# Optimization experiments

Measured on AMD Instinct MI355X. Metric: run time of the kernel, lower is better.

The kernel has to match this reference:

```python
import jax, jax.numpy as jnp
import numpy as np

B, S, D, H = 2, 2048, 1024, 16
HD = D // H
EPS = 1e-5


def _layernorm(x, g, b):
    mu = jnp.mean(x, axis=-1, keepdims=True)
    var = jnp.mean(jnp.square(x - mu), axis=-1, keepdims=True)
    return (x - mu) * jax.lax.rsqrt(var + EPS) * g + b


def setup_inputs() -> dict:
    key = jax.random.key(0)
    ks = jax.random.split(key, 12)
    s = 1.0 / np.sqrt(D)
    return {
        "x": jax.random.normal(ks[0], (B, S, D), jnp.float32),
        "Wq": jax.random.uniform(ks[1], (D, D), jnp.float32, -s, s),
        "bq": jax.random.uniform(ks[2], (D,), jnp.float32, -s, s),
        "Wk": jax.random.uniform(ks[3], (D, D), jnp.float32, -s, s),
        "bk": jax.random.uniform(ks[4], (D,), jnp.float32, -s, s),
        "Wv": jax.random.uniform(ks[5], (D, D), jnp.float32, -s, s),
        "bv": jax.random.uniform(ks[6], (D,), jnp.float32, -s, s),
        "ln_g": jnp.ones((D,), jnp.float32),
        "ln_b": jnp.zeros((D,), jnp.float32),
        "W1": jax.random.uniform(ks[7], (D, D), jnp.float32, -s, s),
        "b1": jax.random.uniform(ks[8], (D,), jnp.float32, -s, s),
        "W2": jax.random.uniform(ks[9], (D, D), jnp.float32, -s, s),
        "b2": jax.random.uniform(ks[10], (D,), jnp.float32, -s, s),
    }


def reference(x, Wq, bq, Wk, bk, Wv, bv, ln_g, ln_b, W1, b1, W2, b2):
    # QKV projections (torch Linear: x @ W.T + b), split into heads -> [B,H,S,HD]
    q = (x @ Wq.T + bq).reshape(B, S, H, HD).transpose(0, 2, 1, 3)
    k = (x @ Wk.T + bk).reshape(B, S, H, HD).transpose(0, 2, 1, 3)
    v = (x @ Wv.T + bv).reshape(B, S, H, HD).transpose(0, 2, 1, 3)
    # Full score matrix [B,H,S,S] (faithful to unfused original)
    scores = jnp.einsum("bhqd,bhkd->bhqk", q, k) / np.sqrt(HD).astype(np.float32)
    attn = jax.nn.softmax(scores, axis=-1)  # dropout = identity (eval mode)
    ctx = jnp.einsum("bhqk,bhkd->bhqd", attn, v)
    ctx = ctx.transpose(0, 2, 1, 3).reshape(B, S, D)
    ctx = _layernorm(ctx + x, ln_g, ln_b)
    ffn = jax.nn.relu(ctx @ W1.T + b1) @ W2.T + b2
    return _layernorm(ffn + ctx, ln_g, ln_b)
```

## Files before the change

### kernel.cpp

```cpp
#include <hip/hip_runtime.h>
#include <stdint.h>

#define D_MODEL 1024
#define NHEAD   16
#define HDIM    64
#define BATCH   2
#define SEQ     2048
#define NTOK    (BATCH*SEQ)

typedef unsigned short u16;
typedef unsigned int   u32;
typedef __attribute__((ext_vector_type(8)))  short bf16x8;
typedef __attribute__((ext_vector_type(8)))  u16   u16x8;
typedef __attribute__((ext_vector_type(4)))  u16   u16x4;
typedef __attribute__((ext_vector_type(4)))  u32   u32x4;
typedef __attribute__((ext_vector_type(4)))  float f32x4;
typedef __attribute__((ext_vector_type(16))) float f32x16;

#if __has_builtin(__builtin_amdgcn_exp2f)
#define EXP2F __builtin_amdgcn_exp2f
#else
#define EXP2F exp2f
#endif

__device__ __forceinline__ u16 f2bf(float f) {
  uint32_t u = __float_as_uint(f);
  u += 0x7fffu + ((u >> 16) & 1u);
  return (u16)(u >> 16);
}

__device__ __forceinline__ void gl_lds16(const u16* g, u16* l) {
  __builtin_amdgcn_global_load_lds(
      (const __attribute__((address_space(1))) void*)g,
      (__attribute__((address_space(3))) void*)l, 16, 0, 0);
}

__device__ __forceinline__ u32 cvtpk(float lo, float hi) {
  u32 r;
  asm("v_cvt_pk_bf16_f32 %0, %1, %2" : "=v"(r) : "v"(lo), "v"(hi));
  return r;
}
__device__ __forceinline__ void pl32swap(u32& a, u32& b) {
  asm("v_permlane32_swap_b32 %0, %1" : "+v"(a), "+v"(b));
}

__device__ __forceinline__ f32x16 mfma32(bf16x8 a, bf16x8 b, f32x16 c) {
  return __builtin_amdgcn_mfma_f32_32x32x16_bf16(a, b, c, 0, 0, 0);
}

__global__ __launch_bounds__(256) void cvt_all(
    const float* __restrict__ x,  const float* __restrict__ Wq,
    const float* __restrict__ Wk, const float* __restrict__ Wv,
    const float* __restrict__ W1, const float* __restrict__ W2,
    const float* __restrict__ bq, const float* __restrict__ bk,
    const float* __restrict__ bv,
    u16* __restrict__ x_bf, u16* __restrict__ wqkv,
    u16* __restrict__ w1b,  u16* __restrict__ w2b,
    float* __restrict__ bqkv) {
  const int bid = blockIdx.x, t = threadIdx.x;
  if (bid == 4608) {
    for (int i = t; i < 3072; i += 256)
      bqkv[i] = i < 1024 ? bq[i] : (i < 2048 ? bk[i - 1024] : bv[i - 2048]);
    return;
  }
  const float* src; u16* dst; int off;
  if (bid < 2048)      { src = x;  dst = x_bf;            off = bid; }
  else if (bid < 2560) { src = Wq; dst = wqkv;            off = bid - 2048; }
  else if (bid < 3072) { src = Wk; dst = wqkv + (1 << 20); off = bid - 2560; }
  else if (bid < 3584) { src = Wv; dst = wqkv + (2 << 20); off = bid - 3072; }
  else if (bid < 4096) { src = W1; dst = w1b;             off = bid - 3584; }
  else                 { src = W2; dst = w2b;             off = bid - 4096; }
  const int i = (off * 256 + t) * 8;
  float4 a = *(const float4*)(src + i);
  float4 b = *(const float4*)(src + i + 4);
  u16x8 o;
  o[0] = f2bf(a.x); o[1] = f2bf(a.y); o[2] = f2bf(a.z); o[3] = f2bf(a.w);
  o[4] = f2bf(b.x); o[5] = f2bf(b.y); o[6] = f2bf(b.z); o[7] = f2bf(b.w);
  *(u16x8*)(dst + i) = o;
}

template <int EPI>
__global__ __launch_bounds__(256) void gemm_bt(const u16* __restrict__ A,
                                               const u16* __restrict__ B,
                                               const float* __restrict__ bias,
                                               void* __restrict__ C,
                                               int M, int N, int K) {
  __shared__ u16 a_lds[128 * 32];
  __shared__ u16 b_lds[128 * 32];
  const int t = threadIdx.x;
  const int l = t & 63;
  const int w = t >> 6;
  const int wr = w >> 1, wc = w & 1;
  const int gxn = N >> 7;
  const int cpx = gridDim.x >> 3;
  const int swz = (blockIdx.x & 7) * cpx + (blockIdx.x >> 3);
  const int bm = (swz / gxn) * 128, bn = (swz % gxn) * 128;
  const int fl = l & 15, fh = l >> 4;

  f32x4 acc[4][4] = {};

  const int row0 = t >> 2;
  const int row1 = (t + 256) >> 2;
  const int col0 = (t & 3) * 8;

  for (int k0 = 0; k0 < K; k0 += 32) {
    __syncthreads();
    gl_lds16(A + (size_t)(bm + row0) * K + k0 + col0, &a_lds[t * 8]);
    gl_lds16(A + (size_t)(bm + row1) * K + k0 + col0, &a_lds[(t + 256) * 8]);
    gl_lds16(B + (size_t)(bn + row0) * K + k0 + col0, &b_lds[t * 8]);
    gl_lds16(B + (size_t)(bn + row1) * K + k0 + col0, &b_lds[(t + 256) * 8]);
    __syncthreads();

    bf16x8 af[4], bf[4];
#pragma unroll
    for (int mi = 0; mi < 4; ++mi)
      af[mi] = *(const bf16x8*)&a_lds[(wr * 64 + mi * 16 + fl) * 32 + fh * 8];
#pragma unroll
    for (int ni = 0; ni < 4; ++ni)
      bf[ni] = *(const bf16x8*)&b_lds[(wc * 64 + ni * 16 + fl) * 32 + fh * 8];
#pragma unroll
    for (int mi = 0; mi < 4; ++mi)
#pragma unroll
      for (int ni = 0; ni < 4; ++ni)
        acc[mi][ni] = __builtin_amdgcn_mfma_f32_16x16x32_bf16(
            af[mi], bf[ni], acc[mi][ni], 0, 0, 0);
  }

#pragma unroll
  for (int mi = 0; mi < 4; ++mi) {
#pragma unroll
    for (int ni = 0; ni < 4; ++ni) {
      const int col = bn + wc * 64 + ni * 16 + fl;
      const float bv = bias ? bias[col] : 0.f;
#pragma unroll
      for (int r = 0; r < 4; ++r) {
        const int row = bm + wr * 64 + mi * 16 + fh * 4 + r;
        float v = acc[mi][ni][r] + bv;
        if (EPI == 0) {
          ((float*)C)[(size_t)row * N + col] = v;
        } else if (EPI == 1) {
          ((u16*)C)[(size_t)row * N + col] = f2bf(v);
        } else {
          ((u16*)C)[(size_t)row * N + col] = f2bf(fmaxf(v, 0.f));
        }
      }
    }
  }
}

__global__ __launch_bounds__(256) void transpose_v(const u16* __restrict__ qkv,
                                                   u16* __restrict__ vT) {
  __shared__ u16 tile[64][72];
  const int t = threadIdx.x;
  const int s0 = blockIdx.x * 64;
  const int bh = blockIdx.y, b = bh >> 4, h = bh & 15;
#pragma unroll
  for (int cc = 0; cc < 2; ++cc) {
    int idx = t + cc * 256, row = idx >> 3, c = idx & 7;
    *(bf16x8*)&tile[row][c * 8] = *(const bf16x8*)(
        qkv + (size_t)(b * SEQ + s0 + row) * 3072 + 2048 + h * 64 + c * 8);
  }
  __syncthreads();
#pragma unroll
  for (int cc = 0; cc < 2; ++cc) {
    int idx = t + cc * 256, drow = idx >> 3, c = idx & 7;
    u16x8 o;
#pragma unroll
    for (int j = 0; j < 8; ++j) o[j] = tile[c * 8 + j][drow];
    *(u16x8*)(vT + (size_t)(bh * 64 + drow) * SEQ + s0 + c * 8) = o;
  }
}

__global__ __launch_bounds__(256, 4) void attn_kernel(const u16* __restrict__ qkv,
                                                      const u16* __restrict__ vT,
                                                      float* __restrict__ ctx) {
  __shared__ u16 smem[4][64 * 64];
  __shared__ float mlbuf[2][2][32][2];

  const int t = threadIdx.x, l = t & 63, w = t >> 6;
  const int r0 = l & 31, hi = l >> 5, hib = hi * 16;
  const int qg = w >> 1, hfv = w & 1;

  const int id = blockIdx.x;
  const int swz = (id & 7) * 128 + (id >> 3);
  const int qblk = swz & 31;
  const int bh = swz >> 5;
  const int b = bh >> 4, h = bh & 15;
  const int q0 = qblk * 64;
  const size_t rowbase = (size_t)b * SEQ;

  bf16x8 qf[4];
#pragma unroll
  for (int kd = 0; kd < 4; ++kd)
    qf[kd] = *(const bf16x8*)(qkv +
        (rowbase + q0 + qg * 32 + r0) * 3072 + h * 64 + kd * 16 + hi * 8);

  f32x16 acc[2] = {};
  float m_run = -1e30f, l_run = 0.f;
  const float C = 0.18033688011f;

  const u16* kb = smem[hfv * 2 + 0];
  const u16* vb = smem[hfv * 2 + 1];

  for (int s = 0; s < 16; ++s) {
    __syncthreads();
#pragma unroll
    for (int cc = 0; cc < 8; ++cc) {
      const int i = t + cc * 256;
      const int arr = i >> 9;
      const int j = i & 511;
      const int rr = j >> 3, cb = (j & 7) * 16;
      const int sc_ = cb ^ ((rr & 7) << 4);
      const int hv = arr >> 1;
      u16* dst = &smem[arr][j * 8];
      if ((arr & 1) == 0)
        gl_lds16(qkv + (rowbase + hv * 1024 + s * 64 + rr) * 3072 + 1024 +
                     h * 64 + (sc_ >> 1), dst);
      else
        gl_lds16(vT + ((size_t)bh * 64 + rr) * SEQ + hv * 1024 + s * 64 +
                     (sc_ >> 1), dst);
    }
    __syncthreads();

    f32x16 p0 = {}, p1 = {};
    __builtin_amdgcn_s_setprio(1);
#pragma unroll
    for (int kd = 0; kd < 4; ++kd) {
      const int cb = kd * 32 + hib;
      const uint8_t* pk = (const uint8_t*)kb;
      bf16x8 klo = *(const bf16x8*)(pk + r0 * 128 + (cb ^ ((r0 & 7) << 4)));
      bf16x8 khi = *(const bf16x8*)(pk + (r0 + 32) * 128 + (cb ^ ((r0 & 7) << 4)));
      p0 = mfma32(klo, qf[kd], p0);
      p1 = mfma32(khi, qf[kd], p1);
    }
    __builtin_amdgcn_s_setprio(0);

    float mx0 = fmaxf(p0[0], p0[1]), mx1 = fmaxf(p0[2], p0[3]);
    float mx2 = fmaxf(p1[0], p1[1]), mx3 = fmaxf(p1[2], p1[3]);
#pragma unroll
    for (int i = 4; i < 16; i += 4) {
      mx0 = fmaxf(mx0, fmaxf(p0[i], p0[i + 1]));
      mx1 = fmaxf(mx1, fmaxf(p0[i + 2], p0[i + 3]));
      mx2 = fmaxf(mx2, fmaxf(p1[i], p1[i + 1]));
      mx3 = fmaxf(mx3, fmaxf(p1[i + 2], p1[i + 3]));
    }
    float mloc = fmaxf(fmaxf(mx0, mx1), fmaxf(mx2, mx3));
    mloc = fmaxf(mloc, __shfl_xor(mloc, 32, 64));

    if (!__all(mloc - m_run <= 44.0f)) {
      const float mnew = fmaxf(m_run, mloc);
      const float sc = EXP2F((m_run - mnew) * C);
      m_run = mnew;
      l_run *= sc;
#pragma unroll
      for (int dblk = 0; dblk < 2; ++dblk)
#pragma unroll
        for (int i = 0; i < 16; ++i) acc[dblk][i] *= sc;
    }
    const float mC = m_run * C;
    float ps = 0.f;
#pragma unroll
    for (int i = 0; i < 16; ++i) {
      p0[i] = EXP2F(fmaf(p0[i], C, -mC));
      ps += p0[i];
    }
#pragma unroll
    for (int i = 0; i < 16; ++i) {
      p1[i] = EXP2F(fmaf(p1[i], C, -mC));
      ps += p1[i];
    }
    ps += __shfl_xor(ps, 32, 64);
    l_run += ps;

    bf16x8 pb[4];
    {
      u32 c0, c1, c2, c3;
      u32x4 f;
      c0 = cvtpk(p0[0], p0[1]);   c1 = cvtpk(p0[2], p0[3]);
      c2 = cvtpk(p0[4], p0[5]);   c3 = cvtpk(p0[6], p0[7]);
      pl32swap(c0, c2); pl32swap(c1, c3);
      f[0] = c0; f[1] = c1; f[2] = c2; f[3] = c3; pb[0] = *(bf16x8*)&f;
      c0 = cvtpk(p0[8], p0[9]);   c1 = cvtpk(p0[10], p0[11]);
      c2 = cvtpk(p0[12], p0[13]); c3 = cvtpk(p0[14], p0[15]);
      pl32swap(c0, c2); pl32swap(c1, c3);
      f[0] = c0; f[1] = c1; f[2] = c2; f[3] = c3; pb[1] = *(bf16x8*)&f;
      c0 = cvtpk(p1[0], p1[1]);   c1 = cvtpk(p1[2], p1[3]);
      c2 = cvtpk(p1[4], p1[5]);   c3 = cvtpk(p1[6], p1[7]);
      pl32swap(c0, c2); pl32swap(c1, c3);
      f[0] = c0; f[1] = c1; f[2] = c2; f[3] = c3; pb[2] = *(bf16x8*)&f;
      c0 = cvtpk(p1[8], p1[9]);   c1 = cvtpk(p1[10], p1[11]);
      c2 = cvtpk(p1[12], p1[13]); c3 = cvtpk(p1[14], p1[15]);
      pl32swap(c0, c2); pl32swap(c1, c3);
      f[0] = c0; f[1] = c1; f[2] = c2; f[3] = c3; pb[3] = *(bf16x8*)&f;
    }

    __builtin_amdgcn_s_setprio(1);
#pragma unroll
    for (int dblk = 0; dblk < 2; ++dblk) {
#pragma unroll
      for (int ks = 0; ks < 4; ++ks) {
        const int rr = dblk * 32 + r0;
        const int cb = ks * 32 + hib;
        bf16x8 vf = *(const bf16x8*)((const uint8_t*)vb + rr * 128 +
                                     (cb ^ ((rr & 7) << 4)));
        acc[dblk] = mfma32(vf, pb[ks], acc[dblk]);
      }
    }
    __builtin_amdgcn_s_setprio(0);
  }

  if (hi == 0) {
    mlbuf[qg][hfv][r0][0] = m_run;
    mlbuf[qg][hfv][r0][1] = l_run;
  }
  __syncthreads();
  const float mo  = mlbuf[qg][hfv ^ 1][r0][0];
  const float lo_ = mlbuf[qg][hfv ^ 1][r0][1];
  const float mM = fmaxf(m_run, mo);
  const float sMine = EXP2F((m_run - mM) * C);
  const float sOth  = EXP2F((mo - mM) * C);
  const float lM = l_run * sMine + lo_ * sOth;

  float* os = (float*)smem + qg * 32 * 68;
  if (hfv == 0) {
#pragma unroll
    for (int dblk = 0; dblk < 2; ++dblk)
#pragma unroll
      for (int i = 0; i < 16; ++i) {
        const int d = dblk * 32 + (i & 3) + 8 * (i >> 2) + 4 * hi;
        os[r0 * 68 + d] = acc[dblk][i] * sMine;
      }
  }
  __syncthreads();
  if (hfv == 1) {
#pragma unroll
    for (int dblk = 0; dblk < 2; ++dblk)
#pragma unroll
      for (int i = 0; i < 16; ++i) {
        const int d = dblk * 32 + (i & 3) + 8 * (i >> 2) + 4 * hi;
        os[r0 * 68 + d] += acc[dblk][i] * sMine;
      }
    if (hi == 0) mlbuf[qg][1][r0][1] = 1.f / lM;
#pragma unroll
    for (int it = 0; it < 8; ++it) {
      const int r = it * 4 + (l >> 4);
      const int c = (l & 15) * 4;
      const float inv = mlbuf[qg][1][r][1];
      float4 v = *(const float4*)&os[r * 68 + c];
      v.x *= inv; v.y *= inv; v.z *= inv; v.w *= inv;
      *(float4*)&ctx[(rowbase + q0 + qg * 32 + r) * D_MODEL + h * 64 + c] = v;
    }
  }
}

__global__ __launch_bounds__(256) void ln_kernel(const float* __restrict__ a,
                                                 const float* __restrict__ res,
                                                 const float* __restrict__ g,
                                                 const float* __restrict__ bta,
                                                 float* __restrict__ outf,
                                                 u16* __restrict__ outb) {
  __shared__ float sbuf[4];
  const int t = threadIdx.x;
  const size_t row = blockIdx.x;
  const float4 va = *(const float4*)(a + row * 1024 + t * 4);
  const float4 vr = *(const float4*)(res + row * 1024 + t * 4);
  float v[4] = {va.x + vr.x, va.y + vr.y, va.z + vr.z, va.w + vr.w};
  float s = v[0] + v[1] + v[2] + v[3];
#pragma unroll
  for (int m = 32; m; m >>= 1) s += __shfl_xor(s, m, 64);
  if ((t & 63) == 0) sbuf[t >> 6] = s;
  __syncthreads();
  const float mean = (sbuf[0] + sbuf[1] + sbuf[2] + sbuf[3]) * (1.f / 1024.f);
  float q = 0.f;
#pragma unroll
  for (int i = 0; i < 4; ++i) { v[i] -= mean; q += v[i] * v[i]; }
#pragma unroll
  for (int m = 32; m; m >>= 1) q += __shfl_xor(q, m, 64);
  __syncthreads();
  if ((t & 63) == 0) sbuf[t >> 6] = q;
  __syncthreads();
  const float var = (sbuf[0] + sbuf[1] + sbuf[2] + sbuf[3]) * (1.f / 1024.f);
  const float rs = rsqrtf(var + 1e-5f);
  const float4 vg = *(const float4*)(g + t * 4);
  const float4 vb = *(const float4*)(bta + t * 4);
  float o[4];
  o[0] = v[0] * rs * vg.x + vb.x;
  o[1] = v[1] * rs * vg.y + vb.y;
  o[2] = v[2] * rs * vg.z + vb.z;
  o[3] = v[3] * rs * vg.w + vb.w;
  float4 of = {o[0], o[1], o[2], o[3]};
  *(float4*)(outf + row * 1024 + t * 4) = of;
  if (outb) {
    u16x4 ob;
#pragma unroll
    for (int i = 0; i < 4; ++i) ob[i] = f2bf(o[i]);
    *(u16x4*)(outb + row * 1024 + t * 4) = ob;
  }
}

extern "C" void kernel_launch(void* const* d_in, const int* in_sizes, int n_in,
                              void* d_out, int out_size, void* d_ws, size_t ws_size,
                              hipStream_t stream) {
  const float* x    = (const float*)d_in[0];
  const float* Wq   = (const float*)d_in[1];
  const float* bq   = (const float*)d_in[2];
  const float* Wk   = (const float*)d_in[3];
  const float* bk   = (const float*)d_in[4];
  const float* Wv   = (const float*)d_in[5];
  const float* bv   = (const float*)d_in[6];
  const float* ln_g = (const float*)d_in[7];
  const float* ln_b = (const float*)d_in[8];
  const float* W1   = (const float*)d_in[9];
  const float* b1   = (const float*)d_in[10];
  const float* W2   = (const float*)d_in[11];
  const float* b2   = (const float*)d_in[12];
  float* out = (float*)d_out;

  uint8_t* ws = (uint8_t*)d_ws;
  const size_t MB = 1 << 20;
  u16*   x_bf  = (u16*)  (ws + 0 * MB);
  u16*   wqkv  = (u16*)  (ws + 8 * MB);
  u16*   w1b   = (u16*)  (ws + 14 * MB);
  u16*   w2b   = (u16*)  (ws + 16 * MB);
  float* bqkv  = (float*)(ws + 18 * MB);
  u16*   qkv   = (u16*)  (ws + 19 * MB);
  u16*   vT    = (u16*)  (ws + 43 * MB);
  float* ctx   = (float*)(ws + 51 * MB);
  float* y     = (float*)(ws + 67 * MB);
  u16*   y_bf  = (u16*)  (ws + 83 * MB);
  u16*   h1    = (u16*)  (ws + 91 * MB);
  float* ffn   = (float*)(ws + 99 * MB);

  cvt_all<<<4609, 256, 0, stream>>>(x, Wq, Wk, Wv, W1, W2, bq, bk, bv,
                                    x_bf, wqkv, w1b, w2b, bqkv);
  gemm_bt<1><<<768, 256, 0, stream>>>(x_bf, wqkv, bqkv, qkv, NTOK, 3072, 1024);
  transpose_v<<<dim3(32, 32), 256, 0, stream>>>(qkv, vT);
  attn_kernel<<<1024, 256, 0, stream>>>(qkv, vT, ctx);
  ln_kernel<<<4096, 256, 0, stream>>>(ctx, x, ln_g, ln_b, y, y_bf);
  gemm_bt<2><<<256, 256, 0, stream>>>(y_bf, w1b, b1, h1, NTOK, 1024, 1024);
  gemm_bt<0><<<256, 256, 0, stream>>>(h1, w2b, b2, ffn, NTOK, 1024, 1024);
  ln_kernel<<<4096, 256, 0, stream>>>(ffn, y, ln_g, ln_b, out, nullptr);
}
```

Baseline: 273.2 us.

## Double-buffer GEMM and attention K tiles, load V fragments directly from global

The GEMM main loop now uses two LDS buffers. The next K-slice is issued before the MFMAs on the current slice, so only one barrier remains per iteration. The attention kernel double-buffers K tiles two steps ahead in LDS and reads V fragments straight from global memory into registers instead of staging them through shared memory. The goal is to overlap global-memory latency with MFMA work and cut barriers. The risks are more register pressure from V fragments held in registers, and less-coalesced per-lane global reads of V.

```diff
diff --git a/kernel.cpp b/kernel.cpp
--- a/kernel.cpp
+++ b/kernel.cpp
@@ -85,8 +85,8 @@
                                                const float* __restrict__ bias,
                                                void* __restrict__ C,
                                                int M, int N, int K) {
-  __shared__ u16 a_lds[128 * 32];
-  __shared__ u16 b_lds[128 * 32];
+  __shared__ u16 a_lds[2][128 * 32];
+  __shared__ u16 b_lds[2][128 * 32];
   const int t = threadIdx.x;
   const int l = t & 63;
   const int w = t >> 6;
@@ -103,28 +103,39 @@
   const int row1 = (t + 256) >> 2;
   const int col0 = (t & 3) * 8;
 
+#define GSTAGE(bb, kk)                                                         \
+  gl_lds16(A + (size_t)(bm + row0) * K + (kk) + col0, &a_lds[bb][t * 8]);      \
+  gl_lds16(A + (size_t)(bm + row1) * K + (kk) + col0,                          \
+           &a_lds[bb][(t + 256) * 8]);                                         \
+  gl_lds16(B + (size_t)(bn + row0) * K + (kk) + col0, &b_lds[bb][t * 8]);      \
+  gl_lds16(B + (size_t)(bn + row1) * K + (kk) + col0,                          \
+           &b_lds[bb][(t + 256) * 8]);
+
+  GSTAGE(0, 0);
+  __syncthreads();
+  int cur = 0;
+
   for (int k0 = 0; k0 < K; k0 += 32) {
-    __syncthreads();
-    gl_lds16(A + (size_t)(bm + row0) * K + k0 + col0, &a_lds[t * 8]);
-    gl_lds16(A + (size_t)(bm + row1) * K + k0 + col0, &a_lds[(t + 256) * 8]);
-    gl_lds16(B + (size_t)(bn + row0) * K + k0 + col0, &b_lds[t * 8]);
-    gl_lds16(B + (size_t)(bn + row1) * K + k0 + col0, &b_lds[(t + 256) * 8]);
-    __syncthreads();
+    if (k0 + 32 < K) { GSTAGE(cur ^ 1, k0 + 32); }
 
     bf16x8 af[4], bf[4];
 #pragma unroll
     for (int mi = 0; mi < 4; ++mi)
-      af[mi] = *(const bf16x8*)&a_lds[(wr * 64 + mi * 16 + fl) * 32 + fh * 8];
+      af[mi] = *(const bf16x8*)&a_lds[cur][(wr * 64 + mi * 16 + fl) * 32 + fh * 8];
 #pragma unroll
     for (int ni = 0; ni < 4; ++ni)
-      bf[ni] = *(const bf16x8*)&b_lds[(wc * 64 + ni * 16 + fl) * 32 + fh * 8];
+      bf[ni] = *(const bf16x8*)&b_lds[cur][(wc * 64 + ni * 16 + fl) * 32 + fh * 8];
 #pragma unroll
     for (int mi = 0; mi < 4; ++mi)
 #pragma unroll
       for (int ni = 0; ni < 4; ++ni)
         acc[mi][ni] = __builtin_amdgcn_mfma_f32_16x16x32_bf16(
             af[mi], bf[ni], acc[mi][ni], 0, 0, 0);
-  }
+
+    __syncthreads();
+    cur ^= 1;
+  }
+#undef GSTAGE
 
 #pragma unroll
   for (int mi = 0; mi < 4; ++mi) {
@@ -174,7 +185,7 @@
 __global__ __launch_bounds__(256, 4) void attn_kernel(const u16* __restrict__ qkv,
                                                       const u16* __restrict__ vT,
                                                       float* __restrict__ ctx) {
-  __shared__ u16 smem[4][64 * 64];
+  __shared__ u16 kset[2][2][64 * 64];
   __shared__ float mlbuf[2][2][32][2];
 
   const int t = threadIdx.x, l = t & 63, w = t >> 6;
@@ -188,6 +199,8 @@
   const int b = bh >> 4, h = bh & 15;
   const int q0 = qblk * 64;
   const size_t rowbase = (size_t)b * SEQ;
+  const size_t vbase = (size_t)bh * 64;
+  const int kvoff = hfv * 1024;
 
   bf16x8 qf[4];
 #pragma unroll
@@ -199,35 +212,41 @@
   float m_run = -1e30f, l_run = 0.f;
   const float C = 0.18033688011f;
 
-  const u16* kb = smem[hfv * 2 + 0];
-  const u16* vb = smem[hfv * 2 + 1];
+#define KSTAGE(bb, ss)                                                         \
+  {                                                                            \
+    _Pragma("unroll")                                                          \
+    for (int cc = 0; cc < 4; ++cc) {                                           \
+      const int i = t + cc * 256;                                              \
+      const int hv = i >> 9, j = i & 511;                                      \
+      const int rr = j >> 3, cb = (j & 7) * 16;                                \
+      const int sc_ = cb ^ ((rr & 7) << 4);                                    \
+      gl_lds16(qkv + (rowbase + hv * 1024 + (ss) * 64 + rr) * 3072 + 1024 +    \
+                   h * 64 + (sc_ >> 1),                                        \
+               &kset[bb][hv][j * 8]);                                          \
+    }                                                                          \
+  }
+
+  KSTAGE(0, 0);
+  KSTAGE(1, 1);
+  __syncthreads();
 
   for (int s = 0; s < 16; ++s) {
-    __syncthreads();
-#pragma unroll
-    for (int cc = 0; cc < 8; ++cc) {
-      const int i = t + cc * 256;
-      const int arr = i >> 9;
-      const int j = i & 511;
-      const int rr = j >> 3, cb = (j & 7) * 16;
-      const int sc_ = cb ^ ((rr & 7) << 4);
-      const int hv = arr >> 1;
-      u16* dst = &smem[arr][j * 8];
-      if ((arr & 1) == 0)
-        gl_lds16(qkv + (rowbase + hv * 1024 + s * 64 + rr) * 3072 + 1024 +
-                     h * 64 + (sc_ >> 1), dst);
-      else
-        gl_lds16(vT + ((size_t)bh * 64 + rr) * SEQ + hv * 1024 + s * 64 +
-                     (sc_ >> 1), dst);
-    }
-    __syncthreads();
+    const int cur = s & 1;
+    const uint8_t* pk = (const uint8_t*)kset[cur][hfv];
+
+    bf16x8 vf[2][4];
+#pragma unroll
+    for (int dblk = 0; dblk < 2; ++dblk)
+#pragma unroll
+      for (int ks = 0; ks < 4; ++ks)
+        vf[dblk][ks] = *(const bf16x8*)(vT + (vbase + dblk * 32 + r0) * SEQ +
+                                        kvoff + s * 64 + ks * 16 + hi * 8);
 
     f32x16 p0 = {}, p1 = {};
     __builtin_amdgcn_s_setprio(1);
 #pragma unroll
     for (int kd = 0; kd < 4; ++kd) {
       const int cb = kd * 32 + hib;
-      const uint8_t* pk = (const uint8_t*)kb;
       bf16x8 klo = *(const bf16x8*)(pk + r0 * 128 + (cb ^ ((r0 & 7) << 4)));
       bf16x8 khi = *(const bf16x8*)(pk + (r0 + 32) * 128 + (cb ^ ((r0 & 7) << 4)));
       p0 = mfma32(klo, qf[kd], p0);
@@ -296,18 +315,16 @@
 
     __builtin_amdgcn_s_setprio(1);
 #pragma unroll
-    for (int dblk = 0; dblk < 2; ++dblk) {
-#pragma unroll
-      for (int ks = 0; ks < 4; ++ks) {
-        const int rr = dblk * 32 + r0;
-        const int cb = ks * 32 + hib;
-        bf16x8 vf = *(const bf16x8*)((const uint8_t*)vb + rr * 128 +
-                                     (cb ^ ((rr & 7) << 4)));
-        acc[dblk] = mfma32(vf, pb[ks], acc[dblk]);
-      }
-    }
+    for (int dblk = 0; dblk < 2; ++dblk)
+#pragma unroll
+      for (int ks = 0; ks < 4; ++ks)
+        acc[dblk] = mfma32(vf[dblk][ks], pb[ks], acc[dblk]);
     __builtin_amdgcn_s_setprio(0);
-  }
+
+    __syncthreads();
+    if (s + 2 < 16) KSTAGE(cur, s + 2);
+  }
+#undef KSTAGE
 
   if (hi == 0) {
     mlbuf[qg][hfv][r0][0] = m_run;
@@ -318,10 +335,9 @@
   const float lo_ = mlbuf[qg][hfv ^ 1][r0][1];
   const float mM = fmaxf(m_run, mo);
   const float sMine = EXP2F((m_run - mM) * C);
-  const float sOth  = EXP2F((mo - mM) * C);
-  const float lM = l_run * sMine + lo_ * sOth;
-
-  float* os = (float*)smem + qg * 32 * 68;
+  const float lM = l_run * sMine + lo_ * EXP2F((mo - mM) * C);
+
+  float* os = (float*)kset + qg * 32 * 68;
   if (hfv == 0) {
 #pragma unroll
     for (int dblk = 0; dblk < 2; ++dblk)
```

After: 327.5 us. 1.2x slower.
